# Kernel optimization log

Hardware: AMD Instinct MI355X
Metric: run time of the kernel (lower is better)

## Reference

```python
import jax, jax.numpy as jnp
import numpy as np
from jax import lax

V_, NC, SPW, H, B, T = 10000, 128, 64, 256, 16, 256  # C = NC*SPW = 8192
NEG = -1e9  # finite stand-in for -inf mask fill (grad-safe)


def _residual(x, w1, b1, w2, b2):
    # ResidualLayerOld: relu(lin2(relu(lin1(x)))) + x  (dropout=0 in eval)
    h = jax.nn.relu(x @ w1 + b1)
    return jax.nn.relu(h @ w2 + b2) + x


def _state_emb(e1, e2):
    # factored state embedding: state (c*SPW + j) -> e1[c] + e2[j]
    return (e1[:, None, :] + e2[None, :, :]).reshape(-1, e1.shape[-1])


def setup_inputs() -> dict:
    key = jax.random.key(0)
    ks = jax.random.split(key, 30)
    w2c = jax.random.randint(ks[0], (V_,), 0, NC)
    # brown-cluster style assignment: each word owns the SPW states of its cluster
    word2state = (w2c[:, None] * SPW + jnp.arange(SPW)[None, :]).astype(jnp.int32)
    text = jax.random.randint(ks[1], (B, T), 0, V_).astype(jnp.int32)

    def n(k, shape, s=0.05):
        return (jax.random.normal(k, shape) * s).astype(jnp.float32)

    z = lambda shape: jnp.zeros(shape, jnp.float32)
    return {
        "text": text, "word2state": word2state,
        "se1_start": n(ks[2], (NC, H), 1.0), "se2_start": n(ks[3], (SPW, H), 1.0),
        "start_w1": n(ks[4], (H, H)), "start_b1": z((H,)),
        "start_w2": n(ks[5], (H, H)), "start_b2": z((H,)),
        "start_pw": n(ks[6], (H, 1)), "start_pb": z((1,)),
        "se1_state": n(ks[7], (NC, H), 1.0), "se2_state": n(ks[8], (SPW, H), 1.0),
        "se1_next": n(ks[9], (NC, H), 1.0), "se2_next": n(ks[10], (SPW, H), 1.0),
        "trans_w1": n(ks[11], (H, H)), "trans_b1": z((H,)),
        "trans_w2": n(ks[12], (H, H)), "trans_b2": z((H,)),
        "se1_pre": n(ks[13], (NC, H), 1.0), "se2_pre": n(ks[14], (SPW, H), 1.0),
        "term_w1": n(ks[15], (H, H)), "term_b1": z((H,)),
        "term_w2": n(ks[16], (H, H)), "term_b2": z((H,)),
        "term_pw": n(ks[17], (H, V_)), "term_pb": z((V_,)),
    }


def reference(text, word2state,
              se1_start, se2_start, start_w1, start_b1, start_w2, start_b2,
              start_pw, start_pb,
              se1_state, se2_state, se1_next, se2_next,
              trans_w1, trans_b1, trans_w2, trans_b2,
              se1_pre, se2_pre, term_w1, term_b1, term_w2, term_b2,
              term_pw, term_pb):
    Vv, k = word2state.shape
    # start distribution over C states
    start_emb = _state_emb(se1_start, se2_start)                       # [C,H]
    start = jax.nn.log_softmax(
        (_residual(start_emb, start_w1, start_b1, start_w2, start_b2) @ start_pw
         + start_pb)[:, 0])                                            # [C]
    # transition: trans_mlp(state_emb) @ next_state_emb.T, row log_softmax
    state_emb = _state_emb(se1_state, se2_state)
    next_emb = _state_emb(se1_next, se2_next)
    transition = jax.nn.log_softmax(
        _residual(state_emb, trans_w1, trans_b1, trans_w2, trans_b2) @ next_emb.T,
        axis=-1)                                                       # [C,C]
    # emission: masked so state c only emits words whose word2state contains c
    pre_emb = _state_emb(se1_pre, se2_pre)
    C = pre_emb.shape[0]
    logits = _residual(pre_emb, term_w1, term_b1, term_w2, term_b2) @ term_pw + term_pb
    mask = jnp.zeros((C, Vv), dtype=bool).at[
        word2state.reshape(-1), jnp.repeat(jnp.arange(Vv), k)].set(True)
    emission = jax.nn.log_softmax(jnp.where(mask, logits, NEG), axis=-1)  # [C,V]
    # clamp to observed words
    cs = word2state[text]                                              # [B,T,k]
    pots = transition[cs[:, :-1, :, None], cs[:, 1:, None, :]]         # [B,T-1,k,k]
    obs = emission[cs, text[:, :, None]]                               # [B,T,k]
    alpha0 = start[cs[:, 0]] + obs[:, 0]                               # [B,k]

    def step(alpha, x):
        pot, o = x  # [B,k,k], [B,k]
        return jax.nn.logsumexp(alpha[:, :, None] + pot, axis=1) + o, None

    alpha, _ = lax.scan(step, alpha0,
                        (jnp.swapaxes(pots, 0, 1), jnp.swapaxes(obs[:, 1:], 0, 1)))
    return jax.nn.logsumexp(alpha, axis=-1)  # log p(text) per batch, [B]
```

## Files before the change

### kernel.cpp

```cpp
#include <hip/hip_runtime.h>
#include <hip/hip_bf16.h>
#include <math.h>

#define HH 256
#define NCC 128
#define SPWW 64
#define CST 8192
#define VV 10000
#define BBB 16
#define TTT 256
#define LOG2E 1.4426950408889634f
#define LN2 0.6931471805599453f

typedef __attribute__((ext_vector_type(8))) short short8;
typedef __attribute__((ext_vector_type(4))) float f32x4;
typedef unsigned short u16;

__device__ inline float bf2f(u16 u) {
    union { unsigned int i; float f; } v; v.i = ((unsigned int)u) << 16; return v.f;
}
__device__ inline u16 f2bf(float f) {
    __hip_bfloat16 h = __float2bfloat16(f);
    return *reinterpret_cast<u16*>(&h);
}
__device__ inline float ex2(float x) { return __builtin_amdgcn_exp2f(x); }
__device__ inline float lg2(float x) { return __builtin_amdgcn_logf(x); }

struct SetupA {
    const float* Ws[6]; u16* Wt;
    const float* pw; u16* pwT;
    const float* e1n; const float* e2n; u16* e1nb; u16* e2nb;
    const int* w2s; int* counts; int* wlist;
    float* startv;
};
__global__ __launch_bounds__(256) void fhmm_setup(SetupA a)
{
    __shared__ float t[64][65];
    int blk = blockIdx.x, tid = threadIdx.x;
    if (blk < 96) {
        int z = blk >> 4, r = blk & 15;
        int k0 = (r & 3) * 64, n0 = (r >> 2) * 64;
        const float* W = a.Ws[z];
        u16* dst = a.Wt + (size_t)z * HH * HH;
        #pragma unroll
        for (int i = 0; i < 16; ++i) {
            int idx = tid + i * 256; int rr = idx >> 6, c = idx & 63;
            t[rr][c] = W[(k0 + rr) * HH + n0 + c];
        }
        __syncthreads();
        #pragma unroll
        for (int i = 0; i < 16; ++i) {
            int idx = tid + i * 256; int rr = idx >> 6, c = idx & 63;
            dst[(n0 + rr) * HH + k0 + c] = f2bf(t[c][rr]);
        }
    } else if (blk < 724) {
        int idx = blk - 96;
        int v0 = (idx % 157) * 64, k0 = (idx / 157) * 64;
        #pragma unroll
        for (int i = 0; i < 16; ++i) {
            int id2 = tid + i * 256; int rr = id2 >> 6, c = id2 & 63;
            int v = v0 + c;
            t[rr][c] = (v < VV) ? a.pw[(size_t)(k0 + rr) * VV + v] : 0.f;
        }
        __syncthreads();
        #pragma unroll
        for (int i = 0; i < 16; ++i) {
            int id2 = tid + i * 256; int rr = id2 >> 6, c = id2 & 63;
            int v = v0 + rr;
            if (v < VV) a.pwT[(size_t)v * HH + k0 + c] = f2bf(t[c][rr]);
        }
    } else if (blk < 852) {
        int idx = (blk - 724) * 256 + tid;
        if (idx < NCC * HH) a.e1nb[idx] = f2bf(a.e1n[idx]);
        if (idx < SPWW * HH) a.e2nb[idx] = f2bf(a.e2n[idx]);
    } else if (blk < 884) {
        int idx = (blk - 852) * 256 + tid;
        if (idx < CST) a.startv[idx] = 0.f;
    } else {
        int c = blk - 884;
        __shared__ int cnt;
        if (tid == 0) cnt = 0;
        __syncthreads();
        for (int v = tid; v < VV; v += 256) {
            if ((a.w2s[v * SPWW] >> 6) == c) {
                int pos = atomicAdd(&cnt, 1);
                a.wlist[c * 256 + pos] = v;
            }
        }
        __syncthreads();
        if (tid == 0) a.counts[c] = cnt;
    }
}

struct MlpA {
    const u16* X[3];
    const float* se1[3]; const float* se2[3];
    const u16* Wth[3];
    const float* bias[3];
    u16* Y[3];
    float oscale[3];
    const float* pw;
    float* startv;
};
template<int LAYER>
__global__ __launch_bounds__(256) void fhmm_mlp_batch(MlpA a)
{
    int hd = blockIdx.z;
    int m0 = blockIdx.x * 64, n0 = blockIdx.y * 64;
    __shared__ char Xs[32768];
    __shared__ char Ws[32768];
    int tid = threadIdx.x, w = tid >> 6, lane = tid & 63, lr = lane & 15, lg = lane >> 4;
    const char* wsrc = (const char*)(a.Wth[hd] + (size_t)n0 * HH);
    if (LAYER == 0) {
        const float* s1 = a.se1[hd];
        const float* s2 = a.se2[hd];
        #pragma unroll
        for (int i = 0; i < 8; ++i) {
            int cc = i * 256 + tid; int row = cc >> 5, tt = cc & 31;
            int gm = m0 + row, k = tt * 8;
            const float* p1 = s1 + (gm >> 6) * HH + k;
            const float* p2 = s2 + (gm & 63) * HH + k;
            u16 pk[8];
            #pragma unroll
            for (int e = 0; e < 8; ++e) pk[e] = f2bf(p1[e] + p2[e]);
            int dst = row * 512 + ((tt ^ (row & 7)) << 4);
            *(uint4*)&Xs[dst] = *(uint4*)pk;
            *(uint4*)&Ws[dst] = *(const uint4*)(wsrc + cc * 16);
        }
    } else {
        const char* xsrc = (const char*)(a.X[hd] + (size_t)m0 * HH);
        #pragma unroll
        for (int i = 0; i < 8; ++i) {
            int cc = i * 256 + tid; int row = cc >> 5, tt = cc & 31;
            int dst = row * 512 + ((tt ^ (row & 7)) << 4);
            *(uint4*)&Xs[dst] = *(const uint4*)(xsrc + cc * 16);
            *(uint4*)&Ws[dst] = *(const uint4*)(wsrc + cc * 16);
        }
    }
    __syncthreads();
    short8 bfr[8];
    int brow = w * 16 + lr, bb = brow * 512, bsw = (brow & 7) << 4;
    #pragma unroll
    for (int ks = 0; ks < 8; ++ks)
        bfr[ks] = *(const short8*)(Ws + bb + (((ks * 4 + lg) << 4) ^ bsw));
    int cb = w * 16 + lg * 4;
    f32x4 bv = *(const f32x4*)(a.bias[hd] + n0 + cb);
    float osc = a.oscale[hd];
    u16* Yp = a.Y[hd];
    #pragma unroll
    for (int rm = 0; rm < 4; ++rm) {
        f32x4 acc = {0.f, 0.f, 0.f, 0.f};
        int ar = rm * 16 + lr, ab = ar * 512, asw = (ar & 7) << 4;
        #pragma unroll
        for (int ks = 0; ks < 8; ++ks) {
            short8 af = *(const short8*)(Xs + ab + (((ks * 4 + lg) << 4) ^ asw));
            acc = __builtin_amdgcn_mfma_f32_16x16x32_bf16(bfr[ks], af, acc, 0, 0, 0);
        }
        int gm = m0 + rm * 16 + lr;
        if (LAYER == 1) {
            const float* r1 = a.se1[hd] + (gm >> 6) * HH + n0 + cb;
            const float* r2 = a.se2[hd] + (gm & 63) * HH + n0 + cb;
            float vals[4];
            #pragma unroll
            for (int e = 0; e < 4; ++e)
                vals[e] = fmaxf(acc[e] + bv[e], 0.f) + r1[e] + r2[e];
            if (hd == 0) {
                const float* pwc = a.pw + n0 + cb;
                float dotp = vals[0] * pwc[0] + vals[1] * pwc[1]
                           + vals[2] * pwc[2] + vals[3] * pwc[3];
                dotp += __shfl_xor(dotp, 16);
                dotp += __shfl_xor(dotp, 32);
                if (lg == 0) atomicAdd(&a.startv[gm], dotp);
            } else {
                ushort4 o;
                #pragma unroll
                for (int e = 0; e < 4; ++e) ((u16*)&o)[e] = f2bf(vals[e] * osc);
                *(ushort4*)(Yp + (size_t)gm * HH + n0 + cb) = o;
            }
        } else {
            ushort4 o;
            #pragma unroll
            for (int e = 0; e < 4; ++e)
                ((u16*)&o)[e] = f2bf(fmaxf(acc[e] + bv[e], 0.f));
            *(ushort4*)(Yp + (size_t)gm * HH + n0 + cb) = o;
        }
    }
}

__global__ __launch_bounds__(256) void fhmm_post(
    const u16* __restrict__ Abf, const u16* __restrict__ e1n,
    const u16* __restrict__ e2n, float* __restrict__ U2, float* __restrict__ V2,
    float* __restrict__ lse_trans2,
    const u16* __restrict__ hpre_bf, const u16* __restrict__ pwT,
    const float* __restrict__ pb, const int* __restrict__ wlist,
    const int* __restrict__ counts,
    float* __restrict__ Ew2, float* __restrict__ lse_em2)
{
    __shared__ char SH[69632];
    int blk = blockIdx.x, tid = threadIdx.x;
    int w = tid >> 6, lane = tid & 63, lr = lane & 15, lg = lane >> 4;

    if (blk < 128) {
        char* Xs = SH;
        char* Ws = SH + 32768;
        float (*lmU)[64] = (float(*)[64])(SH + 65536);
        float (*lsU)[64] = (float(*)[64])(SH + 66560);
        float (*lmV)[64] = (float(*)[64])(SH + 67584);
        float (*lsV)[64] = (float(*)[64])(SH + 68608);
        int m0 = blk * 64;
        const char* xsrc = (const char*)(Abf + (size_t)m0 * HH);
        #pragma unroll
        for (int i = 0; i < 8; ++i) {
            int cc = i * 256 + tid; int row = cc >> 5, tt = cc & 31;
            int dst = row * 512 + ((tt ^ (row & 7)) << 4);
            *(uint4*)&Xs[dst] = *(const uint4*)(xsrc + cc * 16);
        }
        float mU[4], sU[4], mV[4], sV[4];
        #pragma unroll
        for (int rm = 0; rm < 4; ++rm) { mU[rm] = -3e38f; sU[rm] = 0.f; mV[rm] = -3e38f; sV[rm] = 0.f; }
        int cb = w * 16 + lg * 4;
        for (int y = 0; y < 3; ++y) {
            const char* wsrc = (y < 2) ? (const char*)(e1n + (size_t)y * 64 * HH)
                                       : (const char*)e2n;
            __syncthreads();
            #pragma unroll
            for (int i = 0; i < 8; ++i) {
                int cc = i * 256 + tid; int row = cc >> 5, tt = cc & 31;
                int dst = row * 512 + ((tt ^ (row & 7)) << 4);
                *(uint4*)&Ws[dst] = *(const uint4*)(wsrc + cc * 16);
            }
            __syncthreads();
            short8 bfr[8];
            int brow = w * 16 + lr, bb = brow * 512, bsw = (brow & 7) << 4;
            #pragma unroll
            for (int ks = 0; ks < 8; ++ks)
                bfr[ks] = *(const short8*)(Ws + bb + (((ks * 4 + lg) << 4) ^ bsw));
            #pragma unroll
            for (int rm = 0; rm < 4; ++rm) {
                f32x4 acc = {0.f, 0.f, 0.f, 0.f};
                int ar = rm * 16 + lr, ab = ar * 512, asw = (ar & 7) << 4;
                #pragma unroll
                for (int ks = 0; ks < 8; ++ks) {
                    short8 af = *(const short8*)(Xs + ab + (((ks * 4 + lg) << 4) ^ asw));
                    acc = __builtin_amdgcn_mfma_f32_16x16x32_bf16(bfr[ks], af, acc, 0, 0, 0);
                }
                int gm = m0 + rm * 16 + lr;
                float lm = fmaxf(fmaxf(acc[0], acc[1]), fmaxf(acc[2], acc[3]));
                if (y < 2) {
                    *(f32x4*)(U2 + (size_t)gm * NCC + y * 64 + cb) = acc;
                    float mn = fmaxf(mU[rm], lm);
                    sU[rm] = sU[rm] * ex2(mU[rm] - mn)
                           + ex2(acc[0] - mn) + ex2(acc[1] - mn)
                           + ex2(acc[2] - mn) + ex2(acc[3] - mn);
                    mU[rm] = mn;
                } else {
                    *(f32x4*)(V2 + (size_t)gm * SPWW + cb) = acc;
                    float mn = fmaxf(mV[rm], lm);
                    sV[rm] = sV[rm] * ex2(mV[rm] - mn)
                           + ex2(acc[0] - mn) + ex2(acc[1] - mn)
                           + ex2(acc[2] - mn) + ex2(acc[3] - mn);
                    mV[rm] = mn;
                }
            }
        }
        #pragma unroll
        for (int rm = 0; rm < 4; ++rm) {
            #pragma unroll
            for (int d = 16; d < 64; d <<= 1) {
                float m2 = __shfl_xor(mU[rm], d), sx = __shfl_xor(sU[rm], d);
                float mn = fmaxf(mU[rm], m2);
                sU[rm] = sU[rm] * ex2(mU[rm] - mn) + sx * ex2(m2 - mn); mU[rm] = mn;
                m2 = __shfl_xor(mV[rm], d); sx = __shfl_xor(sV[rm], d);
                mn = fmaxf(mV[rm], m2);
                sV[rm] = sV[rm] * ex2(mV[rm] - mn) + sx * ex2(m2 - mn); mV[rm] = mn;
            }
        }
        __syncthreads();
        if (lg == 0) {
            #pragma unroll
            for (int rm = 0; rm < 4; ++rm) {
                lmU[w][rm * 16 + lr] = mU[rm]; lsU[w][rm * 16 + lr] = sU[rm];
                lmV[w][rm * 16 + lr] = mV[rm]; lsV[w][rm * 16 + lr] = sV[rm];
            }
        }
        __syncthreads();
        if (tid < 64) {
            float MU = lmU[0][tid], SU = lsU[0][tid];
            float MV = lmV[0][tid], SV = lsV[0][tid];
            #pragma unroll
            for (int q = 1; q < 4; ++q) {
                float m2 = lmU[q][tid], sx = lsU[q][tid];
                float mn = fmaxf(MU, m2);
                SU = SU * ex2(MU - mn) + sx * ex2(m2 - mn); MU = mn;
                m2 = lmV[q][tid]; sx = lsV[q][tid];
                mn = fmaxf(MV, m2);
                SV = SV * ex2(MV - mn) + sx * ex2(m2 - mn); MV = mn;
            }
            lse_trans2[m0 + tid] = (MU + lg2(SU)) + (MV + lg2(SV));
        }
    } else {
        char* Hs = SH;
        float (*emM)[64] = (float(*)[64])(SH + 32768);
        float (*emS)[64] = (float(*)[64])(SH + 33792);
        int c = blk - 128;
        int cnt = counts[c], off = c * 256;
        const char* src = (const char*)(hpre_bf + (size_t)c * 64 * HH);
        #pragma unroll
        for (int i = 0; i < 8; ++i) {
            int cc = i * 256 + tid; int row = cc >> 5, tt = cc & 31;
            *(uint4*)&Hs[row * 512 + ((tt ^ (row & 7)) << 4)] = *(const uint4*)(src + cc * 16);
        }
        __syncthreads();
        float em_m[4][4], em_s[4][4];
        #pragma unroll
        for (int rm = 0; rm < 4; ++rm)
            #pragma unroll
            for (int e = 0; e < 4; ++e) { em_m[rm][e] = -3e38f; em_s[rm][e] = 0.f; }
        for (int ch = 0; ch * 64 < cnt; ++ch) {
            int widx = ch * 64 + w * 16 + lr;
            bool valid = widx < cnt;
            int v = valid ? wlist[off + widx] : 0;
            short8 bw[8];
            short8 bz = {0, 0, 0, 0, 0, 0, 0, 0};
            #pragma unroll
            for (int ks = 0; ks < 8; ++ks)
                bw[ks] = valid ? *(const short8*)(pwT + (size_t)v * HH + ks * 32 + lg * 8) : bz;
            float pbv = valid ? pb[v] : 0.f;
            #pragma unroll
            for (int rm = 0; rm < 4; ++rm) {
                f32x4 acc = {0.f, 0.f, 0.f, 0.f};
                int ar = rm * 16 + lr, ab = ar * 512, asw = (ar & 7) << 4;
                #pragma unroll
                for (int ks = 0; ks < 8; ++ks) {
                    short8 ah = *(const short8*)(Hs + ab + (((ks * 4 + lg) << 4) ^ asw));
                    acc = __builtin_amdgcn_mfma_f32_16x16x32_bf16(ah, bw[ks], acc, 0, 0, 0);
                }
                f32x4 o;
                #pragma unroll
                for (int e = 0; e < 4; ++e) o[e] = (acc[e] + pbv) * LOG2E;
                if (valid)
                    *(f32x4*)(Ew2 + (size_t)v * 64 + rm * 16 + lg * 4) = o;
                #pragma unroll
                for (int e = 0; e < 4; ++e) {
                    if (valid) {
                        float mn = fmaxf(em_m[rm][e], o[e]);
                        em_s[rm][e] = em_s[rm][e] * ex2(em_m[rm][e] - mn) + ex2(o[e] - mn);
                        em_m[rm][e] = mn;
                    }
                }
            }
        }
        #pragma unroll
        for (int rm = 0; rm < 4; ++rm)
            #pragma unroll
            for (int e = 0; e < 4; ++e) {
                float mm = em_m[rm][e], ss = em_s[rm][e];
                #pragma unroll
                for (int d = 1; d < 16; d <<= 1) {
                    float m2 = __shfl_xor(mm, d);
                    float s2 = __shfl_xor(ss, d);
                    float mn = fmaxf(mm, m2);
                    ss = ss * ex2(mm - mn) + s2 * ex2(m2 - mn);
                    mm = mn;
                }
                em_m[rm][e] = mm; em_s[rm][e] = ss;
            }
        if (lr == 0) {
            #pragma unroll
            for (int rm = 0; rm < 4; ++rm)
                #pragma unroll
                for (int e = 0; e < 4; ++e) {
                    emM[w][rm * 16 + lg * 4 + e] = em_m[rm][e];
                    emS[w][rm * 16 + lg * 4 + e] = em_s[rm][e];
                }
        }
        __syncthreads();
        if (tid < 64) {
            float M = emM[0][tid], S = emS[0][tid];
            #pragma unroll
            for (int q2 = 1; q2 < 4; ++q2) {
                float m2 = emM[q2][tid], s2 = emS[q2][tid];
                float mn = fmaxf(M, m2);
                S = S * ex2(M - mn) + s2 * ex2(m2 - mn); M = mn;
            }
            lse_em2[c * 64 + tid] = M + lg2(fmaxf(S, 1e-33f));
        }
    }
}

template<int LEAF>
__global__ __launch_bounds__(256) void fhmm_combine4(
    const float* __restrict__ U2, const float* __restrict__ V2,
    const float* __restrict__ Ew2, const float* __restrict__ lse_em2,
    const float* __restrict__ lse2,
    const int* __restrict__ text, const int* __restrict__ w2s,
    const float* __restrict__ Lin, float* __restrict__ Lout)
{
    int p = blockIdx.x, b = blockIdx.y;
    int nodes = gridDim.x;
    int tid = threadIdx.x;
    int l6 = tid & 63, q = tid >> 6;

    __shared__ float Rb[64][65];
    __shared__ char Ps[8192], Qs[8192];
    __shared__ float mA2[64], mB2[64], mAf[64], mBf[64];
    __shared__ float part[2][4][64];
    __shared__ float rtB_l[64];

    int nm = LEAF ? ((p == 63) ? 3 : 4) : 4;
    int t0 = 4 * p + 1;
    int in0 = 4 * p;

    float va[16];
    float rowA = 0.f;

    if (LEAF) {
        int vprev = text[b * TTT + (t0 - 1)];
        int vA = text[b * TTT + t0];
        int srA = w2s[vprev * SPWW];
        int sA = w2s[vA * SPWW];
        int cA = sA >> 6;
        rowA = U2[(size_t)(srA + l6) * NCC + cA] - lse2[srA + l6];
        const float* vrow = V2 + (size_t)(srA + l6) * SPWW;
        const float* ewA = Ew2 + (size_t)vA * 64;
        const float* leA = lse_em2 + sA;
        #pragma unroll
        for (int jj = 0; jj < 16; ++jj) {
            int j = q * 16 + jj;
            va[jj] = vrow[j] + ewA[j] - leA[j];
        }
    } else {
        const float* Af = Lin + ((size_t)(b * (4 * nodes) + in0)) * 4096;
        #pragma unroll
        for (int jj = 0; jj < 16; ++jj)
            va[jj] = Af[l6 * 64 + q * 16 + jj];
    }

    for (int s = 1; s < nm; ++s) {
        float mloc = -3e38f;
        #pragma unroll
        for (int jj = 0; jj < 16; ++jj) mloc = fmaxf(mloc, va[jj]);
        part[0][q][l6] = mloc;

        float vb[16], obB = 0.f;
        if (LEAF) {
            int tB = t0 + s;
            int vBp = text[b * TTT + (tB - 1)];
            int vB = text[b * TTT + tB];
            int srB = w2s[vBp * SPWW];
            int sB = w2s[vB * SPWW];
            int cB = sB >> 6;
            if (tid < 64)
                rtB_l[tid] = U2[(size_t)(srB + tid) * NCC + cB] - lse2[srB + tid];
            obB = Ew2[(size_t)vB * 64 + l6] - lse_em2[sB + l6];
            float vraw[16];
            #pragma unroll
            for (int kk = 0; kk < 16; ++kk)
                vraw[kk] = V2[(size_t)(srB + q * 16 + kk) * SPWW + l6];
            __syncthreads();
            float mlocB = -3e38f;
            #pragma unroll
            for (int kk = 0; kk < 16; ++kk) {
                vb[kk] = vraw[kk] + rtB_l[q * 16 + kk];
                mlocB = fmaxf(mlocB, vb[kk]);
            }
            part[1][q][l6] = mlocB;
        } else {
            const float* Bf = Lin + ((size_t)(b * (4 * nodes) + in0 + s)) * 4096;
            float mlocB = -3e38f;
            #pragma unroll
            for (int kk = 0; kk < 16; ++kk) {
                float v = Bf[(q * 16 + kk) * 64 + l6];
                vb[kk] = v; mlocB = fmaxf(mlocB, v);
            }
            part[1][q][l6] = mlocB;
        }
        __syncthreads();

        if (tid < 64) {
            float mf = fmaxf(fmaxf(part[0][0][tid], part[0][1][tid]),
                             fmaxf(part[0][2][tid], part[0][3][tid]));
            mAf[tid] = mf;
            mA2[tid] = mf + ((LEAF && s == 1) ? rowA : 0.f);
        } else if (tid < 128) {
            int j = tid & 63;
            float mf = fmaxf(fmaxf(part[1][0][j], part[1][1][j]),
                             fmaxf(part[1][2][j], part[1][3][j]));
            mBf[j] = mf;
            mB2[j] = mf + obB;
        }
        __syncthreads();

        {
            float ma = mAf[l6];
            u16 pk[16];
            #pragma unroll
            for (int e = 0; e < 16; ++e) pk[e] = f2bf(ex2(va[e] - ma));
            uint4* srcv = (uint4*)pk;
            int base = l6 * 128;
            int s0 = 2 * q, s1 = 2 * q + 1, sw = (l6 & 7);
            *(uint4*)&Ps[base + ((s0 ^ sw) << 4)] = srcv[0];
            *(uint4*)&Ps[base + ((s1 ^ sw) << 4)] = srcv[1];
            float mb = mBf[l6];
            #pragma unroll
            for (int e = 0; e < 16; ++e) pk[e] = f2bf(ex2(vb[e] - mb));
            *(uint4*)&Qs[base + ((s0 ^ sw) << 4)] = srcv[0];
            *(uint4*)&Qs[base + ((s1 ^ sw) << 4)] = srcv[1];
        }
        __syncthreads();

        int w = q, lr = l6 & 15, lg = l6 >> 4;
        int brow = w * 16 + lr;
        short8 bfr[2];
        #pragma unroll
        for (int ks = 0; ks < 2; ++ks)
            bfr[ks] = *(const short8*)(Qs + brow * 128 + (((ks * 4 + lg) << 4) ^ ((brow & 7) << 4)));
        bool last = (s == nm - 1);
        float* Co = Lout + ((size_t)(b * nodes + p)) * 4096;
        #pragma unroll
        for (int rm = 0; rm < 4; ++rm) {
            f32x4 acc = {0.f, 0.f, 0.f, 0.f};
            int ar = rm * 16 + lr;
            #pragma unroll
            for (int ks = 0; ks < 2; ++ks) {
                short8 af = *(const short8*)(Ps + ar * 128 + (((ks * 4 + lg) << 4) ^ ((ar & 7) << 4)));
                acc = __builtin_amdgcn_mfma_f32_16x16x32_bf16(af, bfr[ks], acc, 0, 0, 0);
            }
            #pragma unroll
            for (int e = 0; e < 4; ++e) {
                int ii = rm * 16 + lg * 4 + e;
                int jj = w * 16 + lr;
                float cv = mA2[ii] + mB2[jj] + lg2(fmaxf(acc[e], 1e-33f));
                if (last) Co[ii * 64 + jj] = cv;
                else      Rb[ii][jj] = cv;
            }
        }
        if (!last) {
            __syncthreads();
            #pragma unroll
            for (int jj = 0; jj < 16; ++jj)
                va[jj] = Rb[l6][q * 16 + jj];
        }
    }
}

__global__ __launch_bounds__(256) void fhmm_tree_final(
    const float* __restrict__ Lin,
    const float* __restrict__ startv, const float* __restrict__ Ew2,
    const float* __restrict__ lse_em2,
    const int* __restrict__ text, const int* __restrict__ w2s,
    float* __restrict__ out)
{
    int b = blockIdx.x;
    int tid = threadIdx.x;
    int l6 = tid & 63, q = tid >> 6;

    __shared__ float Rb[64][65];
    __shared__ char Ps[8192], Qs[8192];
    __shared__ float mA2[64], mB2[64], mAf[64], mBf[64];
    __shared__ float part[2][4][64];
    __shared__ float a0[64];
    __shared__ float rm_[4], rs_[4];
    __shared__ float lse_start_s;

    {
        float m = -3e38f, s = 0.f;
        for (int i = tid; i < CST; i += 256) {
            float v = startv[i] * LOG2E;
            float mn = fmaxf(m, v);
            s = s * ex2(m - mn) + ex2(v - mn);
            m = mn;
        }
        #pragma unroll
        for (int d = 32; d; d >>= 1) {
            float m2 = __shfl_xor(m, d), sx = __shfl_xor(s, d);
            float mn = fmaxf(m, m2);
            s = s * ex2(m - mn) + sx * ex2(m2 - mn); m = mn;
        }
        if ((tid & 63) == 0) { rm_[tid >> 6] = m; rs_[tid >> 6] = s; }
        __syncthreads();
        if (tid == 0) {
            float M_ = rm_[0], S_ = rs_[0];
            #pragma unroll
            for (int qq = 1; qq < 4; ++qq) {
                float mn = fmaxf(M_, rm_[qq]);
                S_ = S_ * ex2(M_ - mn) + rs_[qq] * ex2(rm_[qq] - mn); M_ = mn;
            }
            lse_start_s = M_ + lg2(S_);
        }
        __syncthreads();
    }

    float va[16];
    {
        const float* Af = Lin + ((size_t)(b * 4)) * 4096;
        #pragma unroll
        for (int jj = 0; jj < 16; ++jj)
            va[jj] = Af[l6 * 64 + q * 16 + jj];
    }

    for (int s = 1; s < 4; ++s) {
        float mloc = -3e38f;
        #pragma unroll
        for (int jj = 0; jj < 16; ++jj) mloc = fmaxf(mloc, va[jj]);
        part[0][q][l6] = mloc;

        const float* Bf = Lin + ((size_t)(b * 4 + s)) * 4096;
        float vb[16];
        float mlocB = -3e38f;
        #pragma unroll
        for (int kk = 0; kk < 16; ++kk) {
            float v = Bf[(q * 16 + kk) * 64 + l6];
            vb[kk] = v; mlocB = fmaxf(mlocB, v);
        }
        part[1][q][l6] = mlocB;
        __syncthreads();

        if (tid < 64) {
            float mf = fmaxf(fmaxf(part[0][0][tid], part[0][1][tid]),
                             fmaxf(part[0][2][tid], part[0][3][tid]));
            mAf[tid] = mf; mA2[tid] = mf;
        } else if (tid < 128) {
            int j = tid & 63;
            float mf = fmaxf(fmaxf(part[1][0][j], part[1][1][j]),
                             fmaxf(part[1][2][j], part[1][3][j]));
            mBf[j] = mf; mB2[j] = mf;
        }
        __syncthreads();

        {
            float ma = mAf[l6];
            u16 pk[16];
            #pragma unroll
            for (int e = 0; e < 16; ++e) pk[e] = f2bf(ex2(va[e] - ma));
            uint4* srcv = (uint4*)pk;
            int base = l6 * 128;
            int s0 = 2 * q, s1 = 2 * q + 1, sw = (l6 & 7);
            *(uint4*)&Ps[base + ((s0 ^ sw) << 4)] = srcv[0];
            *(uint4*)&Ps[base + ((s1 ^ sw) << 4)] = srcv[1];
            float mb = mBf[l6];
            #pragma unroll
            for (int e = 0; e < 16; ++e) pk[e] = f2bf(ex2(vb[e] - mb));
            *(uint4*)&Qs[base + ((s0 ^ sw) << 4)] = srcv[0];
            *(uint4*)&Qs[base + ((s1 ^ sw) << 4)] = srcv[1];
        }
        __syncthreads();

        int w = q, lr = l6 & 15, lg = l6 >> 4;
        int brow = w * 16 + lr;
        short8 bfr[2];
        #pragma unroll
        for (int ks = 0; ks < 2; ++ks)
            bfr[ks] = *(const short8*)(Qs + brow * 128 + (((ks * 4 + lg) << 4) ^ ((brow & 7) << 4)));
        #pragma unroll
        for (int rm = 0; rm < 4; ++rm) {
            f32x4 acc = {0.f, 0.f, 0.f, 0.f};
            int ar = rm * 16 + lr;
            #pragma unroll
            for (int ks = 0; ks < 2; ++ks) {
                short8 af = *(const short8*)(Ps + ar * 128 + (((ks * 4 + lg) << 4) ^ ((ar & 7) << 4)));
                acc = __builtin_amdgcn_mfma_f32_16x16x32_bf16(af, bfr[ks], acc, 0, 0, 0);
            }
            #pragma unroll
            for (int e = 0; e < 4; ++e) {
                int ii = rm * 16 + lg * 4 + e;
                int jj = w * 16 + lr;
                Rb[ii][jj] = mA2[ii] + mB2[jj] + lg2(fmaxf(acc[e], 1e-33f));
            }
        }
        __syncthreads();
        if (s < 3) {
            #pragma unroll
            for (int jj = 0; jj < 16; ++jj)
                va[jj] = Rb[l6][q * 16 + jj];
        }
    }

    if (tid < 64) {
        int v0 = text[b * TTT];
        int s0 = w2s[v0 * SPWW];
        a0[tid] = startv[s0 + tid] * LOG2E + Ew2[(size_t)v0 * 64 + tid] - lse_em2[s0 + tid];
    }
    __syncthreads();
    float m = -3e38f, s = 0.f;
    for (int e = tid; e < 4096; e += 256) {
        float v = a0[e >> 6] + Rb[e >> 6][e & 63];
        float mn = fmaxf(m, v);
        s = s * ex2(m - mn) + ex2(v - mn);
        m = mn;
    }
    #pragma unroll
    for (int d = 32; d; d >>= 1) {
        float m2 = __shfl_xor(m, d), sx = __shfl_xor(s, d);
        float mn = fmaxf(m, m2);
        s = s * ex2(m - mn) + sx * ex2(m2 - mn); m = mn;
    }
    if ((tid & 63) == 0) { rm_[tid >> 6] = m; rs_[tid >> 6] = s; }
    __syncthreads();
    if (tid == 0) {
        float M_ = rm_[0], S_ = rs_[0];
        #pragma unroll
        for (int qq = 1; qq < 4; ++qq) {
            float mn = fmaxf(M_, rm_[qq]);
            S_ = S_ * ex2(M_ - mn) + rs_[qq] * ex2(rm_[qq] - mn); M_ = mn;
        }
        out[b] = (M_ + lg2(S_) - lse_start_s) * LN2;
    }
}

extern "C" void kernel_launch(void* const* d_in, const int* in_sizes, int n_in,
                              void* d_out, int out_size, void* d_ws, size_t ws_size,
                              hipStream_t stream) {
    const int* text        = (const int*)d_in[0];
    const int* w2s         = (const int*)d_in[1];
    const float* se1_start = (const float*)d_in[2];
    const float* se2_start = (const float*)d_in[3];
    const float* start_w1  = (const float*)d_in[4];
    const float* start_b1  = (const float*)d_in[5];
    const float* start_w2  = (const float*)d_in[6];
    const float* start_b2  = (const float*)d_in[7];
    const float* start_pw  = (const float*)d_in[8];
    const float* start_pb  = (const float*)d_in[9];
    const float* se1_state = (const float*)d_in[10];
    const float* se2_state = (const float*)d_in[11];
    const float* se1_next  = (const float*)d_in[12];
    const float* se2_next  = (const float*)d_in[13];
    const float* trans_w1  = (const float*)d_in[14];
    const float* trans_b1  = (const float*)d_in[15];
    const float* trans_w2  = (const float*)d_in[16];
    const float* trans_b2  = (const float*)d_in[17];
    const float* se1_pre   = (const float*)d_in[18];
    const float* se2_pre   = (const float*)d_in[19];
    const float* term_w1   = (const float*)d_in[20];
    const float* term_b1   = (const float*)d_in[21];
    const float* term_w2   = (const float*)d_in[22];
    const float* term_b2   = (const float*)d_in[23];
    const float* term_pw   = (const float*)d_in[24];
    const float* term_pb   = (const float*)d_in[25];
    float* out = (float*)d_out;

    char* wp = (char*)d_ws;
    auto alloc = [&](size_t bytes) {
        char* p = wp;
        wp += (bytes + 255) & ~(size_t)255;
        return (void*)p;
    };
    u16* h1a         = (u16*)alloc((size_t)CST * HH * 2);
    u16* h1b         = (u16*)alloc((size_t)CST * HH * 2);
    u16* h1c         = (u16*)alloc((size_t)CST * HH * 2);
    u16* h_state_bf  = (u16*)alloc((size_t)CST * HH * 2);
    u16* h_pre_bf    = (u16*)alloc((size_t)CST * HH * 2);
    u16* Wt          = (u16*)alloc((size_t)6 * HH * HH * 2);
    u16* pwT         = (u16*)alloc((size_t)VV * HH * 2);
    u16* e1n_bf      = (u16*)alloc((size_t)NCC * HH * 2);
    u16* e2n_bf      = (u16*)alloc((size_t)SPWW * HH * 2);
    float* U2        = (float*)alloc((size_t)CST * NCC * 4);
    float* V2        = (float*)alloc((size_t)CST * SPWW * 4);
    float* startv    = (float*)alloc(CST * 4);
    float* lse_trans = (float*)alloc(CST * 4);
    float* lse_em    = (float*)alloc(CST * 4);
    float* Ew        = (float*)alloc((size_t)VV * 64 * 4);
    int* counts      = (int*)alloc(NCC * 4);
    int* wlist       = (int*)alloc((size_t)NCC * 256 * 4);
    float* LvA       = (float*)alloc((size_t)BBB * 64 * 4096 * 4);
    float* LvB       = (float*)alloc((size_t)BBB * 16 * 4096 * 4);
    float* LvC       = (float*)alloc((size_t)BBB * 4 * 4096 * 4);
    u16* dummyY      = (u16*)alloc(256 * 2);

    SetupA sa;
    sa.Ws[0] = start_w1; sa.Ws[1] = start_w2; sa.Ws[2] = trans_w1;
    sa.Ws[3] = trans_w2; sa.Ws[4] = term_w1;  sa.Ws[5] = term_w2;
    sa.Wt = Wt; sa.pw = term_pw; sa.pwT = pwT;
    sa.e1n = se1_next; sa.e2n = se2_next; sa.e1nb = e1n_bf; sa.e2nb = e2n_bf;
    sa.w2s = w2s; sa.counts = counts; sa.wlist = wlist;
    sa.startv = startv;
    hipLaunchKernelGGL(fhmm_setup, dim3(1012), 256, 0, stream, sa);

    MlpA m1;
    m1.X[0] = m1.X[1] = m1.X[2] = nullptr;
    m1.se1[0] = se1_start; m1.se1[1] = se1_state; m1.se1[2] = se1_pre;
    m1.se2[0] = se2_start; m1.se2[1] = se2_state; m1.se2[2] = se2_pre;
    m1.Wth[0] = Wt + 0 * HH * HH; m1.Wth[1] = Wt + 2 * HH * HH; m1.Wth[2] = Wt + 4 * HH * HH;
    m1.bias[0] = start_b1; m1.bias[1] = trans_b1; m1.bias[2] = term_b1;
    m1.Y[0] = h1a; m1.Y[1] = h1b; m1.Y[2] = h1c;
    m1.oscale[0] = m1.oscale[1] = m1.oscale[2] = 1.0f;
    m1.pw = start_pw; m1.startv = startv;
    hipLaunchKernelGGL((fhmm_mlp_batch<0>), dim3(128, 4, 3), 256, 0, stream, m1);

    MlpA m2 = m1;
    m2.X[0] = h1a; m2.X[1] = h1b; m2.X[2] = h1c;
    m2.Wth[0] = Wt + 1 * HH * HH; m2.Wth[1] = Wt + 3 * HH * HH; m2.Wth[2] = Wt + 5 * HH * HH;
    m2.bias[0] = start_b2; m2.bias[1] = trans_b2; m2.bias[2] = term_b2;
    m2.Y[0] = dummyY; m2.Y[1] = h_state_bf; m2.Y[2] = h_pre_bf;
    m2.oscale[0] = 1.0f; m2.oscale[1] = LOG2E; m2.oscale[2] = 1.0f;
    hipLaunchKernelGGL((fhmm_mlp_batch<1>), dim3(128, 4, 3), 256, 0, stream, m2);

    hipLaunchKernelGGL(fhmm_post, dim3(256), 256, 0, stream,
                       h_state_bf, e1n_bf, e2n_bf, U2, V2, lse_trans,
                       h_pre_bf, pwT, term_pb, wlist, counts, Ew, lse_em);

    hipLaunchKernelGGL((fhmm_combine4<1>), dim3(64, BBB), 256, 0, stream,
                       U2, V2, Ew, lse_em, lse_trans, text, w2s,
                       (const float*)nullptr, LvA);
    hipLaunchKernelGGL((fhmm_combine4<0>), dim3(16, BBB), 256, 0, stream,
                       (const float*)nullptr, (const float*)nullptr,
                       (const float*)nullptr, (const float*)nullptr,
                       (const float*)nullptr, (const int*)nullptr,
                       (const int*)nullptr, LvA, LvB);
    hipLaunchKernelGGL((fhmm_combine4<0>), dim3(4, BBB), 256, 0, stream,
                       (const float*)nullptr, (const float*)nullptr,
                       (const float*)nullptr, (const float*)nullptr,
                       (const float*)nullptr, (const int*)nullptr,
                       (const int*)nullptr, LvB, LvC);

    hipLaunchKernelGGL(fhmm_tree_final, dim3(BBB), 256, 0, stream,
                       LvC, startv, Ew, lse_em, text, w2s, out);
}
```

Measured before the change: 109.0 us.

## Fuse both MLP layers into one kernel and use radix-8 tree combine

The two residual-MLP layers for all three heads now run in one kernel. Each block computes a 64-row tile through layer 1, keeps the hidden activations in shared memory, then applies layer 2, so the three intermediate hidden buffers are no longer written to and read back from global memory. Weights are read straight from global memory instead of being staged in LDS. Separately, the log-space chain reduction tree now combines 8 steps per node instead of 4, dropping one combine launch. The cost is fewer, longer-running blocks (384 instead of 1536 for the MLP) and more serial work per combine block.

```diff
diff --git a/kernel.cpp b/kernel.cpp
--- a/kernel.cpp
+++ b/kernel.cpp
@@ -92,26 +92,24 @@
     }
 }
 
-struct MlpA {
-    const u16* X[3];
+struct MlpF {
     const float* se1[3]; const float* se2[3];
-    const u16* Wth[3];
-    const float* bias[3];
+    const u16* W1t[3]; const u16* W2t[3];
+    const float* b1[3]; const float* b2[3];
     u16* Y[3];
     float oscale[3];
     const float* pw;
     float* startv;
 };
-template<int LAYER>
-__global__ __launch_bounds__(256) void fhmm_mlp_batch(MlpA a)
+__global__ __launch_bounds__(256, 2) void fhmm_mlp_fused(MlpF a)
 {
-    int hd = blockIdx.z;
-    int m0 = blockIdx.x * 64, n0 = blockIdx.y * 64;
+    int hd = blockIdx.y;
+    int m0 = blockIdx.x * 64;
     __shared__ char Xs[32768];
-    __shared__ char Ws[32768];
+    __shared__ char Hs[32768];
     int tid = threadIdx.x, w = tid >> 6, lane = tid & 63, lr = lane & 15, lg = lane >> 4;
-    const char* wsrc = (const char*)(a.Wth[hd] + (size_t)n0 * HH);
-    if (LAYER == 0) {
+
+    {
         const float* s1 = a.se1[hd];
         const float* s2 = a.se2[hd];
         #pragma unroll
@@ -123,66 +121,94 @@
             u16 pk[8];
             #pragma unroll
             for (int e = 0; e < 8; ++e) pk[e] = f2bf(p1[e] + p2[e]);
-            int dst = row * 512 + ((tt ^ (row & 7)) << 4);
-            *(uint4*)&Xs[dst] = *(uint4*)pk;
-            *(uint4*)&Ws[dst] = *(const uint4*)(wsrc + cc * 16);
-        }
-    } else {
-        const char* xsrc = (const char*)(a.X[hd] + (size_t)m0 * HH);
-        #pragma unroll
-        for (int i = 0; i < 8; ++i) {
-            int cc = i * 256 + tid; int row = cc >> 5, tt = cc & 31;
-            int dst = row * 512 + ((tt ^ (row & 7)) << 4);
-            *(uint4*)&Xs[dst] = *(const uint4*)(xsrc + cc * 16);
-            *(uint4*)&Ws[dst] = *(const uint4*)(wsrc + cc * 16);
+            *(uint4*)&Xs[row * 512 + ((tt ^ (row & 7)) << 4)] = *(uint4*)pk;
         }
     }
     __syncthreads();
-    short8 bfr[8];
-    int brow = w * 16 + lr, bb = brow * 512, bsw = (brow & 7) << 4;
-    #pragma unroll
-    for (int ks = 0; ks < 8; ++ks)
-        bfr[ks] = *(const short8*)(Ws + bb + (((ks * 4 + lg) << 4) ^ bsw));
-    int cb = w * 16 + lg * 4;
-    f32x4 bv = *(const f32x4*)(a.bias[hd] + n0 + cb);
-    float osc = a.oscale[hd];
-    u16* Yp = a.Y[hd];
-    #pragma unroll
-    for (int rm = 0; rm < 4; ++rm) {
-        f32x4 acc = {0.f, 0.f, 0.f, 0.f};
-        int ar = rm * 16 + lr, ab = ar * 512, asw = (ar & 7) << 4;
-        #pragma unroll
-        for (int ks = 0; ks < 8; ++ks) {
-            short8 af = *(const short8*)(Xs + ab + (((ks * 4 + lg) << 4) ^ asw));
-            acc = __builtin_amdgcn_mfma_f32_16x16x32_bf16(bfr[ks], af, acc, 0, 0, 0);
-        }
-        int gm = m0 + rm * 16 + lr;
-        if (LAYER == 1) {
-            const float* r1 = a.se1[hd] + (gm >> 6) * HH + n0 + cb;
-            const float* r2 = a.se2[hd] + (gm & 63) * HH + n0 + cb;
-            float vals[4];
-            #pragma unroll
-            for (int e = 0; e < 4; ++e)
-                vals[e] = fmaxf(acc[e] + bv[e], 0.f) + r1[e] + r2[e];
-            if (hd == 0) {
-                const float* pwc = a.pw + n0 + cb;
-                float dotp = vals[0] * pwc[0] + vals[1] * pwc[1]
-                           + vals[2] * pwc[2] + vals[3] * pwc[3];
-                dotp += __shfl_xor(dotp, 16);
-                dotp += __shfl_xor(dotp, 32);
-                if (lg == 0) atomicAdd(&a.startv[gm], dotp);
-            } else {
-                ushort4 o;
-                #pragma unroll
-                for (int e = 0; e < 4; ++e) ((u16*)&o)[e] = f2bf(vals[e] * osc);
-                *(ushort4*)(Yp + (size_t)gm * HH + n0 + cb) = o;
-            }
-        } else {
-            ushort4 o;
-            #pragma unroll
-            for (int e = 0; e < 4; ++e)
-                ((u16*)&o)[e] = f2bf(fmaxf(acc[e] + bv[e], 0.f));
-            *(ushort4*)(Yp + (size_t)gm * HH + n0 + cb) = o;
+
+    {
+        const u16* W1 = a.W1t[hd];
+        const float* b1 = a.b1[hd];
+        int brow = w * 16 + lr;
+        for (int nt = 0; nt < 4; ++nt) {
+            int n0 = nt * 64;
+            short8 bfr[8];
+            #pragma unroll
+            for (int ks = 0; ks < 8; ++ks)
+                bfr[ks] = *(const short8*)(W1 + (size_t)(n0 + brow) * HH + ks * 32 + lg * 8);
+            int cb = w * 16 + lg * 4;
+            f32x4 bv = *(const f32x4*)(b1 + n0 + cb);
+            #pragma unroll
+            for (int rm = 0; rm < 4; ++rm) {
+                f32x4 acc = {0.f, 0.f, 0.f, 0.f};
+                int ar = rm * 16 + lr, ab = ar * 512, asw = (ar & 7) << 4;
+                #pragma unroll
+                for (int ks = 0; ks < 8; ++ks) {
+                    short8 af = *(const short8*)(Xs + ab + (((ks * 4 + lg) << 4) ^ asw));
+                    acc = __builtin_amdgcn_mfma_f32_16x16x32_bf16(bfr[ks], af, acc, 0, 0, 0);
+                }
+                u16 pk[4];
+                #pragma unroll
+                for (int e = 0; e < 4; ++e) pk[e] = f2bf(fmaxf(acc[e] + bv[e], 0.f));
+                int c2 = (n0 + cb) * 2;
+                int slot = c2 >> 4;
+                *(uint2*)&Hs[ar * 512 + ((slot ^ (ar & 7)) << 4) + (c2 & 15)] = *(uint2*)pk;
+            }
+        }
+    }
+    __syncthreads();
+
+    {
+        const u16* W2 = a.W2t[hd];
+        const float* b2 = a.b2[hd];
+        float osc = a.oscale[hd];
+        u16* Yp = a.Y[hd];
+        int brow = w * 16 + lr;
+        int cbl = w * 16 + lg * 4;
+        float dotp[4] = {0.f, 0.f, 0.f, 0.f};
+        for (int nt = 0; nt < 4; ++nt) {
+            int n0 = nt * 64;
+            short8 bfr[8];
+            #pragma unroll
+            for (int ks = 0; ks < 8; ++ks)
+                bfr[ks] = *(const short8*)(W2 + (size_t)(n0 + brow) * HH + ks * 32 + lg * 8);
+            f32x4 bv = *(const f32x4*)(b2 + n0 + cbl);
+            #pragma unroll
+            for (int rm = 0; rm < 4; ++rm) {
+                f32x4 acc = {0.f, 0.f, 0.f, 0.f};
+                int ar = rm * 16 + lr, ab = ar * 512, asw = (ar & 7) << 4;
+                #pragma unroll
+                for (int ks = 0; ks < 8; ++ks) {
+                    short8 af = *(const short8*)(Hs + ab + (((ks * 4 + lg) << 4) ^ asw));
+                    acc = __builtin_amdgcn_mfma_f32_16x16x32_bf16(bfr[ks], af, acc, 0, 0, 0);
+                }
+                int gm = m0 + rm * 16 + lr;
+                const float* r1 = a.se1[hd] + (gm >> 6) * HH + n0 + cbl;
+                const float* r2 = a.se2[hd] + (gm & 63) * HH + n0 + cbl;
+                float vals[4];
+                #pragma unroll
+                for (int e = 0; e < 4; ++e)
+                    vals[e] = fmaxf(acc[e] + bv[e], 0.f) + r1[e] + r2[e];
+                if (hd == 0) {
+                    const float* pwc = a.pw + n0 + cbl;
+                    dotp[rm] += vals[0] * pwc[0] + vals[1] * pwc[1]
+                              + vals[2] * pwc[2] + vals[3] * pwc[3];
+                } else {
+                    ushort4 o;
+                    #pragma unroll
+                    for (int e = 0; e < 4; ++e) ((u16*)&o)[e] = f2bf(vals[e] * osc);
+                    *(ushort4*)(Yp + (size_t)gm * HH + n0 + cbl) = o;
+                }
+            }
+        }
+        if (hd == 0) {
+            #pragma unroll
+            for (int rm = 0; rm < 4; ++rm) {
+                float d = dotp[rm];
+                d += __shfl_xor(d, 16);
+                d += __shfl_xor(d, 32);
+                if (lg == 0) atomicAdd(&a.startv[m0 + rm * 16 + lr], d);
+            }
         }
     }
 }
@@ -389,7 +415,7 @@
 }
 
 template<int LEAF>
-__global__ __launch_bounds__(256) void fhmm_combine4(
+__global__ __launch_bounds__(256) void fhmm_combine8(
     const float* __restrict__ U2, const float* __restrict__ V2,
     const float* __restrict__ Ew2, const float* __restrict__ lse_em2,
     const float* __restrict__ lse2,
@@ -407,9 +433,9 @@
     __shared__ float part[2][4][64];
     __shared__ float rtB_l[64];
 
-    int nm = LEAF ? ((p == 63) ? 3 : 4) : 4;
-    int t0 = 4 * p + 1;
-    int in0 = 4 * p;
+    int nm = LEAF ? ((p == 31) ? 7 : 8) : 8;
+    int t0 = 8 * p + 1;
+    int in0 = 8 * p;
 
     float va[16];
     float rowA = 0.f;
@@ -430,7 +456,7 @@
             va[jj] = vrow[j] + ewA[j] - leA[j];
         }
     } else {
-        const float* Af = Lin + ((size_t)(b * (4 * nodes) + in0)) * 4096;
+        const float* Af = Lin + ((size_t)(b * 32 + in0)) * 4096;
         #pragma unroll
         for (int jj = 0; jj < 16; ++jj)
             va[jj] = Af[l6 * 64 + q * 16 + jj];
@@ -466,7 +492,7 @@
             }
             part[1][q][l6] = mlocB;
         } else {
-            const float* Bf = Lin + ((size_t)(b * (4 * nodes) + in0 + s)) * 4096;
+            const float* Bf = Lin + ((size_t)(b * 32 + in0 + s)) * 4096;
             float mlocB = -3e38f;
             #pragma unroll
             for (int kk = 0; kk < 16; ++kk) {
@@ -745,9 +771,6 @@
         wp += (bytes + 255) & ~(size_t)255;
         return (void*)p;
     };
-    u16* h1a         = (u16*)alloc((size_t)CST * HH * 2);
-    u16* h1b         = (u16*)alloc((size_t)CST * HH * 2);
-    u16* h1c         = (u16*)alloc((size_t)CST * HH * 2);
     u16* h_state_bf  = (u16*)alloc((size_t)CST * HH * 2);
     u16* h_pre_bf    = (u16*)alloc((size_t)CST * HH * 2);
     u16* Wt          = (u16*)alloc((size_t)6 * HH * HH * 2);
@@ -762,8 +785,7 @@
     float* Ew        = (float*)alloc((size_t)VV * 64 * 4);
     int* counts      = (int*)alloc(NCC * 4);
     int* wlist       = (int*)alloc((size_t)NCC * 256 * 4);
-    float* LvA       = (float*)alloc((size_t)BBB * 64 * 4096 * 4);
-    float* LvB       = (float*)alloc((size_t)BBB * 16 * 4096 * 4);
+    float* LvA       = (float*)alloc((size_t)BBB * 32 * 4096 * 4);
     float* LvC       = (float*)alloc((size_t)BBB * 4 * 4096 * 4);
     u16* dummyY      = (u16*)alloc(256 * 2);
 
@@ -776,42 +798,30 @@
     sa.startv = startv;
     hipLaunchKernelGGL(fhmm_setup, dim3(1012), 256, 0, stream, sa);
 
-    MlpA m1;
-    m1.X[0] = m1.X[1] = m1.X[2] = nullptr;
-    m1.se1[0] = se1_start; m1.se1[1] = se1_state; m1.se1[2] = se1_pre;
-    m1.se2[0] = se2_start; m1.se2[1] = se2_state; m1.se2[2] = se2_pre;
-    m1.Wth[0] = Wt + 0 * HH * HH; m1.Wth[1] = Wt + 2 * HH * HH; m1.Wth[2] = Wt + 4 * HH * HH;
-    m1.bias[0] = start_b1; m1.bias[1] = trans_b1; m1.bias[2] = term_b1;
-    m1.Y[0] = h1a; m1.Y[1] = h1b; m1.Y[2] = h1c;
-    m1.oscale[0] = m1.oscale[1] = m1.oscale[2] = 1.0f;
-    m1.pw = start_pw; m1.startv = startv;
-    hipLaunchKernelGGL((fhmm_mlp_batch<0>), dim3(128, 4, 3), 256, 0, stream, m1);
-
-    MlpA m2 = m1;
-    m2.X[0] = h1a; m2.X[1] = h1b; m2.X[2] = h1c;
-    m2.Wth[0] = Wt + 1 * HH * HH; m2.Wth[1] = Wt + 3 * HH * HH; m2.Wth[2] = Wt + 5 * HH * HH;
-    m2.bias[0] = start_b2; m2.bias[1] = trans_b2; m2.bias[2] = term_b2;
-    m2.Y[0] = dummyY; m2.Y[1] = h_state_bf; m2.Y[2] = h_pre_bf;
-    m2.oscale[0] = 1.0f; m2.oscale[1] = LOG2E; m2.oscale[2] = 1.0f;
-    hipLaunchKernelGGL((fhmm_mlp_batch<1>), dim3(128, 4, 3), 256, 0, stream, m2);
+    MlpF mf;
+    mf.se1[0] = se1_start; mf.se1[1] = se1_state; mf.se1[2] = se1_pre;
+    mf.se2[0] = se2_start; mf.se2[1] = se2_state; mf.se2[2] = se2_pre;
+    mf.W1t[0] = Wt + 0 * HH * HH; mf.W1t[1] = Wt + 2 * HH * HH; mf.W1t[2] = Wt + 4 * HH * HH;
+    mf.W2t[0] = Wt + 1 * HH * HH; mf.W2t[1] = Wt + 3 * HH * HH; mf.W2t[2] = Wt + 5 * HH * HH;
+    mf.b1[0] = start_b1; mf.b1[1] = trans_b1; mf.b1[2] = term_b1;
+    mf.b2[0] = start_b2; mf.b2[1] = trans_b2; mf.b2[2] = term_b2;
+    mf.Y[0] = dummyY; mf.Y[1] = h_state_bf; mf.Y[2] = h_pre_bf;
+    mf.oscale[0] = 1.0f; mf.oscale[1] = LOG2E; mf.oscale[2] = 1.0f;
+    mf.pw = start_pw; mf.startv = startv;
+    hipLaunchKernelGGL(fhmm_mlp_fused, dim3(128, 3), 256, 0, stream, mf);
 
     hipLaunchKernelGGL(fhmm_post, dim3(256), 256, 0, stream,
                        h_state_bf, e1n_bf, e2n_bf, U2, V2, lse_trans,
                        h_pre_bf, pwT, term_pb, wlist, counts, Ew, lse_em);
 
-    hipLaunchKernelGGL((fhmm_combine4<1>), dim3(64, BBB), 256, 0, stream,
+    hipLaunchKernelGGL((fhmm_combine8<1>), dim3(32, BBB), 256, 0, stream,
                        U2, V2, Ew, lse_em, lse_trans, text, w2s,
                        (const float*)nullptr, LvA);
-    hipLaunchKernelGGL((fhmm_combine4<0>), dim3(16, BBB), 256, 0, stream,
+    hipLaunchKernelGGL((fhmm_combine8<0>), dim3(4, BBB), 256, 0, stream,
                        (const float*)nullptr, (const float*)nullptr,
                        (const float*)nullptr, (const float*)nullptr,
                        (const float*)nullptr, (const int*)nullptr,
-                       (const int*)nullptr, LvA, LvB);
-    hipLaunchKernelGGL((fhmm_combine4<0>), dim3(4, BBB), 256, 0, stream,
-                       (const float*)nullptr, (const float*)nullptr,
-                       (const float*)nullptr, (const float*)nullptr,
-                       (const float*)nullptr, (const int*)nullptr,
-                       (const int*)nullptr, LvB, LvC);
+                       (const int*)nullptr, LvA, LvC);
 
     hipLaunchKernelGGL(fhmm_tree_final, dim3(BBB), 256, 0, stream,
                        LvC, startv, Ew, lse_em, text, w2s, out);
```

Result: no change. 110.0 us (+0.9%).
